# Kernel tuning notes

Measured on AMD Instinct MI355X. Metric: run time of the kernel, lower is better.

Reference implementation:

```python
import jax, jax.numpy as jnp
import numpy as np

B, N, R, OUT = 8192, 4096, 16, 4096
STD = 0.01


def setup_inputs() -> dict:
    key = jax.random.key(0)
    ks = jax.random.split(key, 6)
    x = jax.random.normal(ks[0], (B, N), dtype=jnp.float32)
    G = STD * jax.random.normal(ks[1], (R, N), dtype=jnp.float32)
    H = STD * jax.random.normal(ks[2], (R, N), dtype=jnp.float32)
    b1 = STD * jax.random.normal(ks[3], (N,), dtype=jnp.float32)
    W2 = STD * jax.random.normal(ks[4], (N, OUT), dtype=jnp.float32)
    b2 = STD * jax.random.normal(ks[5], (OUT,), dtype=jnp.float32)
    return {"x": x, "G": G, "H": H, "b1": b1, "W2": W2, "b2": b2}


def reference(x, G, H, b1, W2, b2):
    # low-rank structured layer: xW = (x @ H^T) @ G  -- rank-r factorization of W
    xH = jnp.einsum('bn,rn->br', x, H)   # [B, r]
    xW = jnp.einsum('br,rn->bn', xH, G)  # [B, N]
    h = jax.nn.relu(xW + b1)             # num_layers == 1 branch
    y = jnp.matmul(h, W2) + b2           # [B, OUT]
    return y
```

## Files before the change

kernel.cpp:

```cpp
#include <hip/hip_runtime.h>
#include <hip/hip_bf16.h>
#include <cstdint>
#include <cstddef>

typedef __bf16 bf16;
typedef __bf16 bf16x4 __attribute__((ext_vector_type(4)));
typedef __bf16 bf16x8 __attribute__((ext_vector_type(8)));
typedef float  f32x4  __attribute__((ext_vector_type(4)));
typedef float  f32x8  __attribute__((ext_vector_type(8)));

#define MB   8192
#define NN   4096
#define RR   16
#define KOUT 4096

#define FENCE() asm volatile("" ::: "memory")
#define BARRIER() do { FENCE(); __builtin_amdgcn_s_barrier(); FENCE(); } while (0)

__device__ __forceinline__ void gload_lds16(const bf16* g, bf16* l) {
  __builtin_amdgcn_global_load_lds(
      (const __attribute__((address_space(1))) void*)g,
      (__attribute__((address_space(3))) void*)l, 16, 0, 0);
}

__global__ __launch_bounds__(256) void f_pre(
    const float* __restrict__ x, const float* __restrict__ H,
    const float* __restrict__ G, const float* __restrict__ b1,
    bf16* __restrict__ hout,
    const float* __restrict__ W2, bf16* __restrict__ W2t)
{
  __shared__ float red[4][64][4];
  __shared__ float sS[16][16];
  __shared__ float tile[64][65];
  const int t = threadIdx.x;

  if (blockIdx.x < 512) {
    const int lane = t & 63, w = t >> 6;
    const int r0 = blockIdx.x * 16;
    const int fr = lane & 15, fk = lane >> 4;

    const float* xp = x + (size_t)(r0 + fr) * NN + w * 1024 + fk * 8;
    const float* hp = H + (size_t)fr * NN + w * 1024 + fk * 8;

    f32x4 acc = {0.f, 0.f, 0.f, 0.f};
#pragma unroll 4
    for (int c = 0; c < 32; ++c) {
      const f32x4 xa = *(const f32x4*)(xp + c * 32);
      const f32x4 xb = *(const f32x4*)(xp + c * 32 + 4);
      const f32x4 ha = *(const f32x4*)(hp + c * 32);
      const f32x4 hb = *(const f32x4*)(hp + c * 32 + 4);
      bf16x8 af, bfv;
#pragma unroll
      for (int j = 0; j < 4; ++j) {
        af[j] = (bf16)xa[j]; af[4 + j] = (bf16)xb[j];
        bfv[j] = (bf16)ha[j]; bfv[4 + j] = (bf16)hb[j];
      }
      acc = __builtin_amdgcn_mfma_f32_16x16x32_bf16(af, bfv, acc, 0, 0, 0);
    }
    *(f32x4*)&red[w][lane][0] = acc;
    __syncthreads();
    if (t < 64) {
      f32x4 s = *(const f32x4*)&red[0][t][0];
      s += *(const f32x4*)&red[1][t][0];
      s += *(const f32x4*)&red[2][t][0];
      s += *(const f32x4*)&red[3][t][0];
#pragma unroll
      for (int q = 0; q < 4; ++q)
        sS[(t >> 4) * 4 + q][t & 15] = s[q];
    }
    __syncthreads();

#pragma unroll
    for (int half = 0; half < 2; ++half) {
      const int col = half * 2048 + t * 8;
      const f32x8 bv = *(const f32x8*)(b1 + col);
#pragma unroll
      for (int rg = 0; rg < 4; ++rg) {
        f32x8 a0 = bv, a1 = bv, a2 = bv, a3 = bv;
#pragma unroll
        for (int r = 0; r < 16; ++r) {
          const f32x8 g8 = *(const f32x8*)(G + (size_t)r * NN + col);
          a0 += sS[rg * 4 + 0][r] * g8;
          a1 += sS[rg * 4 + 1][r] * g8;
          a2 += sS[rg * 4 + 2][r] * g8;
          a3 += sS[rg * 4 + 3][r] * g8;
        }
#define STORE_ROW(jj, av) {                                            \
        bf16x8 o;                                                      \
        _Pragma("unroll")                                              \
        for (int j = 0; j < 8; ++j) o[j] = (bf16)fmaxf((av)[j], 0.f);  \
        *(bf16x8*)(hout + (size_t)(r0 + rg * 4 + (jj)) * NN + col) = o; }
        STORE_ROW(0, a0) STORE_ROW(1, a1) STORE_ROW(2, a2) STORE_ROW(3, a3)
#undef STORE_ROW
      }
    }
  } else {
    const int bid  = blockIdx.x - 512;
    const int kb   = (bid >> 6) * 64;
    const int ob   = (bid & 63) * 64;
    const int row  = t >> 4;
    const int col4 = (t & 15) * 4;
#pragma unroll
    for (int p = 0; p < 4; ++p) {
      const f32x4 v = *(const f32x4*)(W2 + (size_t)(kb + p*16 + row) * KOUT + ob + col4);
      tile[p*16 + row][col4 + 0] = v[0];
      tile[p*16 + row][col4 + 1] = v[1];
      tile[p*16 + row][col4 + 2] = v[2];
      tile[p*16 + row][col4 + 3] = v[3];
    }
    __syncthreads();
    const int jj0 = t >> 4;
    const int ii4 = (t & 15) * 4;
#pragma unroll
    for (int p = 0; p < 4; ++p) {
      const int jj = p*16 + jj0;
      bf16x4 o;
      o[0] = (bf16)tile[ii4 + 0][jj];
      o[1] = (bf16)tile[ii4 + 1][jj];
      o[2] = (bf16)tile[ii4 + 2][jj];
      o[3] = (bf16)tile[ii4 + 3][jj];
      *(bf16x4*)(W2t + (size_t)(ob + jj) * NN + kb + ii4) = o;
    }
  }
}

#define NT 64

__global__ __launch_bounds__(512, 1) void k3_gemm256(
    const bf16* __restrict__ A, const bf16* __restrict__ Bt,
    const float* __restrict__ b2, float* __restrict__ C)
{
  extern __shared__ __align__(16) char smem[];
  bf16* lds = (bf16*)smem;
  const char* ldsc = (const char*)smem;

  const int bid = blockIdx.x;
  const int swz = (bid & 7) * 64 + (bid >> 3);
  const int tm = swz >> 4, tn = swz & 15;
  const int brow = tm * 256, bcol = tn * 256;

  const int t    = threadIdx.x;
  const int lane = t & 63;
  const int wave = t >> 6;
  const int wr   = wave >> 2;
  const int wc   = wave & 3;
  const int fr   = lane & 15;
  const int fk   = lane >> 4;

  int srow[2], scol[2];
#pragma unroll
  for (int i = 0; i < 2; ++i) {
    const int d   = i * 8192 + t * 16;
    const int row = d >> 7;
    const int l   = d ^ ((row & 7) << 4);
    srow[i] = row;
    scol[i] = (l & 127) >> 1;
  }
  const bf16* gA0 = A  + (size_t)brow * NN;
  const bf16* gA1 = A  + (size_t)(brow + 128) * NN;
  const bf16* gB0 = Bt + (size_t)bcol * NN;
  const bf16* gB1 = Bt + (size_t)(bcol + 128) * NN;

  auto stage = [&](const bf16* g, int regionElem, int kt) {
#pragma unroll
    for (int i = 0; i < 2; ++i)
      gload_lds16(g + (size_t)srow[i] * NN + kt + scol[i],
                  lds + regionElem + i * 4096 + t * 8);
  };

  auto offA = [&](int mi, int kk) -> int {
    const int row = mi * 32 + wr * 16 + fr;
    const int b = row * 128 + kk * 64 + fk * 16;
    return b ^ ((row & 7) << 4);
  };
  auto offB = [&](int nj, int kk) -> int {
    const int row = nj * 64 + wc * 16 + fr;
    const int b = row * 128 + kk * 64 + fk * 16;
    return b ^ ((row & 7) << 4);
  };

  f32x4 acc[8][4];
#pragma unroll
  for (int m = 0; m < 8; ++m)
#pragma unroll
    for (int n = 0; n < 4; ++n) acc[m][n] = (f32x4){0.f,0.f,0.f,0.f};

  bf16x8 a[8], b0[4], b1[4];

  stage(gA0, 0,           0); stage(gB0, 32768,       0);
  stage(gB1, 32768+8192,  0); stage(gA1, 8192,        0);
  stage(gA0, 16384,       64); stage(gB0, 32768+16384, 64);
  stage(gB1, 32768+16384+8192, 64);
  asm volatile("s_waitcnt vmcnt(6)" ::: "memory");
  BARRIER();
#pragma unroll
  for (int mi = 0; mi < 4; ++mi)
#pragma unroll
    for (int kk = 0; kk < 2; ++kk)
      a[mi*2+kk] = *(const bf16x8*)(ldsc + offA(mi, kk));
#pragma unroll
  for (int nj = 0; nj < 2; ++nj)
#pragma unroll
    for (int kk = 0; kk < 2; ++kk)
      b0[nj*2+kk] = *(const bf16x8*)(ldsc + 65536 + offB(nj, kk));

#pragma unroll 1
  for (int u0 = 0; u0 < NT; u0 += 2) {
#pragma unroll
    for (int hi = 0; hi < 2; ++hi) {
      const int u   = u0 + hi;
      const int buf = hi;
      const int obuf = buf ^ 1;
      const char* pa  = ldsc + buf  * 32768;
      const char* pb  = ldsc + 65536 + buf  * 32768;
      const char* pan = ldsc + obuf * 32768;
      const char* pbn = ldsc + 65536 + obuf * 32768;

      if (u < NT-1) stage(gA1, obuf*16384 + 8192, (u+1)*64);
      __builtin_amdgcn_s_setprio(1);
#pragma unroll
      for (int mi = 0; mi < 4; ++mi)
#pragma unroll
        for (int nj = 0; nj < 2; ++nj)
#pragma unroll
          for (int kk = 0; kk < 2; ++kk)
            acc[mi][nj] = __builtin_amdgcn_mfma_f32_16x16x32_bf16(
                a[mi*2+kk], b0[nj*2+kk], acc[mi][nj], 0, 0, 0);
#pragma unroll
      for (int nj = 0; nj < 2; ++nj)
#pragma unroll
        for (int kk = 0; kk < 2; ++kk)
          b1[nj*2+kk] = *(const bf16x8*)(pb + 16384 + offB(nj, kk));
      __builtin_amdgcn_s_setprio(0);

      BARRIER();
      if (u < NT-2) stage(gA0, buf*16384, (u+2)*64);
      __builtin_amdgcn_s_setprio(1);
#pragma unroll
      for (int mi = 0; mi < 4; ++mi)
#pragma unroll
        for (int nj = 0; nj < 2; ++nj)
#pragma unroll
          for (int kk = 0; kk < 2; ++kk)
            acc[mi][2+nj] = __builtin_amdgcn_mfma_f32_16x16x32_bf16(
                a[mi*2+kk], b1[nj*2+kk], acc[mi][2+nj], 0, 0, 0);
#pragma unroll
      for (int mi = 0; mi < 4; ++mi)
#pragma unroll
        for (int kk = 0; kk < 2; ++kk)
          a[mi*2+kk] = *(const bf16x8*)(pa + 16384 + offA(mi, kk));
      __builtin_amdgcn_s_setprio(0);

      if (u < NT-2) stage(gB0, 32768 + buf*16384, (u+2)*64);
      __builtin_amdgcn_s_setprio(1);
#pragma unroll
      for (int mi = 0; mi < 4; ++mi)
#pragma unroll
        for (int nj = 0; nj < 2; ++nj)
#pragma unroll
          for (int kk = 0; kk < 2; ++kk)
            acc[4+mi][2+nj] = __builtin_amdgcn_mfma_f32_16x16x32_bf16(
                a[mi*2+kk], b1[nj*2+kk], acc[4+mi][2+nj], 0, 0, 0);
      __builtin_amdgcn_s_setprio(0);

      if (u < NT-2) stage(gB1, 32768 + buf*16384 + 8192, (u+2)*64);
      if (u < NT-2)       { asm volatile("s_waitcnt vmcnt(6)" ::: "memory"); }
      else if (u == NT-2) { asm volatile("s_waitcnt vmcnt(0)" ::: "memory"); }
      BARRIER();
      __builtin_amdgcn_s_setprio(1);
#pragma unroll
      for (int mi = 0; mi < 4; ++mi)
#pragma unroll
        for (int nj = 0; nj < 2; ++nj)
#pragma unroll
          for (int kk = 0; kk < 2; ++kk)
            acc[4+mi][nj] = __builtin_amdgcn_mfma_f32_16x16x32_bf16(
                a[mi*2+kk], b0[nj*2+kk], acc[4+mi][nj], 0, 0, 0);
      if (u < NT-1) {
#pragma unroll
        for (int mi = 0; mi < 4; ++mi)
#pragma unroll
          for (int kk = 0; kk < 2; ++kk)
            a[mi*2+kk] = *(const bf16x8*)(pan + offA(mi, kk));
#pragma unroll
        for (int nj = 0; nj < 2; ++nj)
#pragma unroll
          for (int kk = 0; kk < 2; ++kk)
            b0[nj*2+kk] = *(const bf16x8*)(pbn + offB(nj, kk));
      }
      __builtin_amdgcn_s_setprio(0);
      BARRIER();
    }
  }

#pragma unroll
  for (int n = 0; n < 4; ++n) {
    const int col = bcol + n * 64 + wc * 16 + fr;
    const float bias = b2[col];
#pragma unroll
    for (int m = 0; m < 8; ++m) {
      const int row0 = brow + m * 32 + wr * 16 + fk * 4;
      float* cp = C + (size_t)row0 * KOUT + col;
#pragma unroll
      for (int q = 0; q < 4; ++q)
        cp[(size_t)q * KOUT] = acc[m][n][q] + bias;
    }
  }
}

extern "C" void kernel_launch(void* const* d_in, const int* in_sizes, int n_in,
                              void* d_out, int out_size, void* d_ws, size_t ws_size,
                              hipStream_t stream) {
  const float* x  = (const float*)d_in[0];
  const float* G  = (const float*)d_in[1];
  const float* H  = (const float*)d_in[2];
  const float* b1 = (const float*)d_in[3];
  const float* W2 = (const float*)d_in[4];
  const float* b2 = (const float*)d_in[5];
  float* y = (float*)d_out;

  bf16* hbuf = (bf16*)d_ws;
  bf16* w2t  = hbuf + (size_t)MB * NN;

  hipFuncSetAttribute((const void*)k3_gemm256,
                      hipFuncAttributeMaxDynamicSharedMemorySize, 131072);

  hipLaunchKernelGGL(f_pre, dim3(512 + 64 * 64), dim3(256), 0, stream,
                     x, H, G, b1, hbuf, W2, w2t);
  hipLaunchKernelGGL(k3_gemm256, dim3((MB/256) * (KOUT/256)), dim3(512), 131072,
                     stream, hbuf, w2t, b2, y);
}
```

Before: 305.1 us.

## Use fp32 dot products for x@H^T with 4-row blocks and drop GEMM loop barrier

The low-rank projection now uses plain fp32 vector dot products, with each block handling 4 rows instead of 16. This quadruples the preprocessing grid and drops the bf16 conversion and MFMA path. Separately, the trailing barrier at the end of each k-iteration of the main GEMM is removed, which cuts synchronisation cost. Without that barrier, LDS buffers may be overwritten while other waves are still reading them, so results could race.

```diff
diff --git a/kernel.cpp b/kernel.cpp
--- a/kernel.cpp
+++ b/kernel.cpp
@@ -23,90 +23,72 @@
       (__attribute__((address_space(3))) void*)l, 16, 0, 0);
 }
 
-__global__ __launch_bounds__(256) void f_pre(
+__global__ __launch_bounds__(256) void d_pre(
     const float* __restrict__ x, const float* __restrict__ H,
     const float* __restrict__ G, const float* __restrict__ b1,
     bf16* __restrict__ hout,
     const float* __restrict__ W2, bf16* __restrict__ W2t)
 {
-  __shared__ float red[4][64][4];
-  __shared__ float sS[16][16];
+  __shared__ float red[4][64];
+  __shared__ float sS[4][16];
   __shared__ float tile[64][65];
   const int t = threadIdx.x;
 
-  if (blockIdx.x < 512) {
+  if (blockIdx.x < 2048) {
+    const int r0   = blockIdx.x * 4;
     const int lane = t & 63, w = t >> 6;
-    const int r0 = blockIdx.x * 16;
-    const int fr = lane & 15, fk = lane >> 4;
-
-    const float* xp = x + (size_t)(r0 + fr) * NN + w * 1024 + fk * 8;
-    const float* hp = H + (size_t)fr * NN + w * 1024 + fk * 8;
-
-    f32x4 acc = {0.f, 0.f, 0.f, 0.f};
-#pragma unroll 4
-    for (int c = 0; c < 32; ++c) {
-      const f32x4 xa = *(const f32x4*)(xp + c * 32);
-      const f32x4 xb = *(const f32x4*)(xp + c * 32 + 4);
-      const f32x4 ha = *(const f32x4*)(hp + c * 32);
-      const f32x4 hb = *(const f32x4*)(hp + c * 32 + 4);
-      bf16x8 af, bfv;
-#pragma unroll
-      for (int j = 0; j < 4; ++j) {
-        af[j] = (bf16)xa[j]; af[4 + j] = (bf16)xb[j];
-        bfv[j] = (bf16)ha[j]; bfv[4 + j] = (bf16)hb[j];
-      }
-      acc = __builtin_amdgcn_mfma_f32_16x16x32_bf16(af, bfv, acc, 0, 0, 0);
-    }
-    *(f32x4*)&red[w][lane][0] = acc;
+    const int row  = lane >> 4;
+    const int r    = lane & 15;
+    const float* xp = x + (size_t)(r0 + row) * NN + w * 1024;
+    const float* hp = H + (size_t)r * NN + w * 1024;
+
+    f32x4 acc4 = {0.f, 0.f, 0.f, 0.f};
+#pragma unroll 8
+    for (int k = 0; k < 1024; k += 4) {
+      const f32x4 xv = *(const f32x4*)(xp + k);
+      const f32x4 hv = *(const f32x4*)(hp + k);
+      acc4 += xv * hv;
+    }
+    red[w][lane] = acc4[0] + acc4[1] + acc4[2] + acc4[3];
     __syncthreads();
-    if (t < 64) {
-      f32x4 s = *(const f32x4*)&red[0][t][0];
-      s += *(const f32x4*)&red[1][t][0];
-      s += *(const f32x4*)&red[2][t][0];
-      s += *(const f32x4*)&red[3][t][0];
-#pragma unroll
-      for (int q = 0; q < 4; ++q)
-        sS[(t >> 4) * 4 + q][t & 15] = s[q];
-    }
+    if (t < 64)
+      sS[t >> 4][t & 15] = red[0][t] + red[1][t] + red[2][t] + red[3][t];
     __syncthreads();
 
 #pragma unroll
     for (int half = 0; half < 2; ++half) {
       const int col = half * 2048 + t * 8;
       const f32x8 bv = *(const f32x8*)(b1 + col);
-#pragma unroll
-      for (int rg = 0; rg < 4; ++rg) {
-        f32x8 a0 = bv, a1 = bv, a2 = bv, a3 = bv;
-#pragma unroll
-        for (int r = 0; r < 16; ++r) {
-          const f32x8 g8 = *(const f32x8*)(G + (size_t)r * NN + col);
-          a0 += sS[rg * 4 + 0][r] * g8;
-          a1 += sS[rg * 4 + 1][r] * g8;
-          a2 += sS[rg * 4 + 2][r] * g8;
-          a3 += sS[rg * 4 + 3][r] * g8;
-        }
-#define STORE_ROW(jj, av) {                                            \
-        bf16x8 o;                                                      \
-        _Pragma("unroll")                                              \
-        for (int j = 0; j < 8; ++j) o[j] = (bf16)fmaxf((av)[j], 0.f);  \
-        *(bf16x8*)(hout + (size_t)(r0 + rg * 4 + (jj)) * NN + col) = o; }
-        STORE_ROW(0, a0) STORE_ROW(1, a1) STORE_ROW(2, a2) STORE_ROW(3, a3)
+      f32x8 a0 = bv, a1 = bv, a2 = bv, a3 = bv;
+#pragma unroll
+      for (int rr = 0; rr < 16; ++rr) {
+        const f32x8 g8 = *(const f32x8*)(G + (size_t)rr * NN + col);
+        a0 += sS[0][rr] * g8;
+        a1 += sS[1][rr] * g8;
+        a2 += sS[2][rr] * g8;
+        a3 += sS[3][rr] * g8;
+      }
+#define STORE_ROW(jj, av) {                                          \
+      bf16x8 o;                                                      \
+      _Pragma("unroll")                                              \
+      for (int j = 0; j < 8; ++j) o[j] = (bf16)fmaxf((av)[j], 0.f);  \
+      *(bf16x8*)(hout + (size_t)(r0 + (jj)) * NN + col) = o; }
+      STORE_ROW(0, a0) STORE_ROW(1, a1) STORE_ROW(2, a2) STORE_ROW(3, a3)
 #undef STORE_ROW
-      }
     }
   } else {
-    const int bid  = blockIdx.x - 512;
+    const int bid  = blockIdx.x - 2048;
     const int kb   = (bid >> 6) * 64;
     const int ob   = (bid & 63) * 64;
-    const int row  = t >> 4;
+    const int rowi = t >> 4;
     const int col4 = (t & 15) * 4;
 #pragma unroll
     for (int p = 0; p < 4; ++p) {
-      const f32x4 v = *(const f32x4*)(W2 + (size_t)(kb + p*16 + row) * KOUT + ob + col4);
-      tile[p*16 + row][col4 + 0] = v[0];
-      tile[p*16 + row][col4 + 1] = v[1];
-      tile[p*16 + row][col4 + 2] = v[2];
-      tile[p*16 + row][col4 + 3] = v[3];
+      const f32x4 v = *(const f32x4*)(W2 + (size_t)(kb + p*16 + rowi) * KOUT + ob + col4);
+      tile[p*16 + rowi][col4 + 0] = v[0];
+      tile[p*16 + rowi][col4 + 1] = v[1];
+      tile[p*16 + rowi][col4 + 2] = v[2];
+      tile[p*16 + rowi][col4 + 3] = v[3];
     }
     __syncthreads();
     const int jj0 = t >> 4;
@@ -289,7 +271,6 @@
             b0[nj*2+kk] = *(const bf16x8*)(pbn + offB(nj, kk));
       }
       __builtin_amdgcn_s_setprio(0);
-      BARRIER();
     }
   }
 
@@ -325,7 +306,7 @@
   hipFuncSetAttribute((const void*)k3_gemm256,
                       hipFuncAttributeMaxDynamicSharedMemorySize, 131072);
 
-  hipLaunchKernelGGL(f_pre, dim3(512 + 64 * 64), dim3(256), 0, stream,
+  hipLaunchKernelGGL(d_pre, dim3(2048 + 4096), dim3(256), 0, stream,
                      x, H, G, b1, hbuf, W2, w2t);
   hipLaunchKernelGGL(k3_gemm256, dim3((MB/256) * (KOUT/256)), dim3(512), 131072,
                      stream, hbuf, w2t, b2, y);
```

Result: slower. 508.3 us (+66.6%).
